# Optimization experiments

Measured on AMD Instinct MI355X. Metric: run time of the kernel, lower is better.

The kernel has to match this reference:

```python
import jax, jax.numpy as jnp
import numpy as np

B, N, E = 2, 2048, 1024   # batch, seq_len, embed_dim (= hidden_dim)
H, HD = 16, 64            # num_heads, head_dim


def setup_inputs() -> dict:
    key = jax.random.key(0)
    ks = jax.random.split(key, 6)
    w = lambda k: jax.random.normal(k, (E, E), jnp.float32) * 0.02
    return {
        "x": jax.random.normal(ks[0], (B, N, E), jnp.float32),
        "Wq": w(ks[1]), "bq": jnp.zeros((E,), jnp.float32),
        "Wk": w(ks[2]), "bk": jnp.zeros((E,), jnp.float32),
        "Wv": w(ks[3]), "bv": jnp.zeros((E,), jnp.float32),
        "Wu": w(ks[4]), "bu": jnp.zeros((E,), jnp.float32),
        "Wo": w(ks[5]), "bo": jnp.zeros((E,), jnp.float32),
        "ln_g": jnp.ones((E,), jnp.float32),
        "ln_b": jnp.zeros((E,), jnp.float32),
    }


def reference(x, Wq, bq, Wk, bk, Wv, bv, Wu, bu, Wo, bo, ln_g, ln_b):
    # projections (torch Linear: x @ W.T + b)
    q = x @ Wq.T + bq
    k = x @ Wk.T + bk
    v = jax.nn.silu(x @ Wv.T + bv)   # uv_act = swish
    u = jax.nn.silu(x @ Wu.T + bu)
    # split heads: [B, N, H*HD] -> [B, H, N, HD]
    split = lambda t: t.reshape(B, N, H, HD).transpose(0, 2, 1, 3)
    q, k, v = split(q), split(k), split(v)
    # non-softmax attention: ReLU on scaled energy (no causal mask)
    energy = jnp.einsum("bhnd,bhmd->bhnm", q, k) / jnp.float32(np.sqrt(HD))
    energy = jax.nn.relu(energy)
    out = jnp.einsum("bhnm,bhmd->bhnd", energy, v)
    # merge heads: [B, H, N, HD] -> [B, N, H*HD]
    out = out.transpose(0, 2, 1, 3).reshape(B, N, H * HD)
    # layernorm over hidden_dim
    mu = out.mean(-1, keepdims=True)
    var = out.var(-1, keepdims=True)
    out = (out - mu) * jax.lax.rsqrt(var + 1e-5) * ln_g + ln_b
    # gate and output projection
    out = u * out
    return out @ Wo.T + bo
```

## Files before the change

### kernel.cpp

```cpp
#include <hip/hip_runtime.h>
#include <stdint.h>

typedef unsigned short u16;
typedef __attribute__((ext_vector_type(8))) short short8;
typedef __attribute__((ext_vector_type(4))) short short4v;
typedef __attribute__((ext_vector_type(4))) float floatx4;
typedef __attribute__((ext_vector_type(4))) int intx4;

#define B_ 2
#define N_ 2048
#define E_ 1024
#define H_ 16
#define HD_ 64
#define M_TOT (B_ * N_)

__device__ __forceinline__ float bf2f(u16 h) {
    union { unsigned u; float f; } c; c.u = ((unsigned)h) << 16; return c.f;
}
__device__ __forceinline__ u16 f2bf(float f) {
    union { float f; unsigned u; } c; c.f = f;
    unsigned r = c.u + 0x7FFFu + ((c.u >> 16) & 1u);
    return (u16)(r >> 16);
}
__device__ __forceinline__ float silu_f(float x) { return x / (1.f + __expf(-x)); }

template <typename T> __device__ __forceinline__ void store_out(T* p, float v);
template <> __device__ __forceinline__ void store_out<u16>(u16* p, float v)    { *p = f2bf(v); }
template <> __device__ __forceinline__ void store_out<float>(float* p, float v) { *p = v; }

__device__ __forceinline__ void gll16(const void* g, void* l) {
    __builtin_amdgcn_global_load_lds(
        (const __attribute__((address_space(1))) void*)g,
        (__attribute__((address_space(3))) void*)l,
        16, 0, 0);
}

__launch_bounds__(256, 4)
__global__ void cvt_bf16(const float* __restrict__ src, u16* __restrict__ dst, int n)
{
    const int i = (blockIdx.x * 256 + threadIdx.x) * 8;
    if (i >= n) return;
    floatx4 a = *(const floatx4*)(src + i);
    floatx4 b = *(const floatx4*)(src + i + 4);
    union { u16 h[8]; intx4 v; } o;
    o.h[0] = f2bf(a[0]); o.h[1] = f2bf(a[1]); o.h[2] = f2bf(a[2]); o.h[3] = f2bf(a[3]);
    o.h[4] = f2bf(b[0]); o.h[5] = f2bf(b[1]); o.h[6] = f2bf(b[2]); o.h[7] = f2bf(b[3]);
    *(intx4*)(dst + i) = o.v;
}

__launch_bounds__(256, 4)
__global__ void cvt5(const float* __restrict__ s0, const float* __restrict__ s1,
                     const float* __restrict__ s2, const float* __restrict__ s3,
                     const float* __restrict__ s4,
                     u16* __restrict__ d0, u16* __restrict__ d1,
                     u16* __restrict__ d2, u16* __restrict__ d3,
                     u16* __restrict__ d4)
{
    const int z = blockIdx.z;
    const float* src = (z == 0) ? s0 : (z == 1) ? s1 : (z == 2) ? s2 : (z == 3) ? s3 : s4;
    u16* dst         = (z == 0) ? d0 : (z == 1) ? d1 : (z == 2) ? d2 : (z == 3) ? d3 : d4;
    const int i = (blockIdx.x * 256 + threadIdx.x) * 8;
    floatx4 a = *(const floatx4*)(src + i);
    floatx4 b = *(const floatx4*)(src + i + 4);
    union { u16 h[8]; intx4 v; } o;
    o.h[0] = f2bf(a[0]); o.h[1] = f2bf(a[1]); o.h[2] = f2bf(a[2]); o.h[3] = f2bf(a[3]);
    o.h[4] = f2bf(b[0]); o.h[5] = f2bf(b[1]); o.h[6] = f2bf(b[2]); o.h[7] = f2bf(b[3]);
    *(intx4*)(dst + i) = o.v;
}

template <typename OutT>
__launch_bounds__(256, 2)
__global__ void gemm4(const u16* __restrict__ A,
                      const u16* __restrict__ W0, const u16* __restrict__ W1,
                      const u16* __restrict__ W2, const u16* __restrict__ W3,
                      const float* __restrict__ bi0, const float* __restrict__ bi1,
                      const float* __restrict__ bi2, const float* __restrict__ bi3,
                      OutT* __restrict__ O0, OutT* __restrict__ O1,
                      OutT* __restrict__ O2, OutT* __restrict__ O3,
                      int actmask, int K)
{
    __shared__ u16 a_lds[128 * 32];
    __shared__ u16 b_lds[128 * 32];

    const int z = blockIdx.z;
    const u16* W    = (z == 0) ? W0 : (z == 1) ? W1 : (z == 2) ? W2 : W3;
    const float* Bi = (z == 0) ? bi0 : (z == 1) ? bi1 : (z == 2) ? bi2 : bi3;
    OutT* Out       = (z == 0) ? O0 : (z == 1) ? O1 : (z == 2) ? O2 : O3;
    const bool act = (actmask >> z) & 1;

    const int t    = threadIdx.x;
    const int wave = t >> 6, lane = t & 63, quad = lane >> 4, l16 = lane & 15;
    const int wm = wave >> 1, wn = wave & 1;
    const int m0 = blockIdx.y * 128;
    const int n0 = blockIdx.x * 128;

    floatx4 acc[4][4];
    const floatx4 fz = {0.f, 0.f, 0.f, 0.f};
    for (int i = 0; i < 4; i++)
        for (int j = 0; j < 4; j++) acc[i][j] = fz;

    const int ar = t >> 2;
    const int ac = (t & 3) * 8;
    const u16* Ag0 = A + (size_t)(m0 + ar) * K + ac;
    const u16* Ag1 = A + (size_t)(m0 + 64 + ar) * K + ac;
    const u16* Bg0 = W + (size_t)(n0 + ar) * K + ac;
    const u16* Bg1 = W + (size_t)(n0 + 64 + ar) * K + ac;
    u16* al0 = a_lds + wave * 512;
    u16* al1 = a_lds + 2048 + wave * 512;
    u16* bl0 = b_lds + wave * 512;
    u16* bl1 = b_lds + 2048 + wave * 512;

    for (int k0 = 0; k0 < K; k0 += 32) {
        __syncthreads();
        gll16(Ag0 + k0, al0);
        gll16(Ag1 + k0, al1);
        gll16(Bg0 + k0, bl0);
        gll16(Bg1 + k0, bl1);
        __syncthreads();

        short8 af[4], bfr[4];
        for (int i = 0; i < 4; i++)
            af[i]  = *(const short8*)&a_lds[(wm * 64 + i * 16 + l16) * 32 + quad * 8];
        for (int j = 0; j < 4; j++)
            bfr[j] = *(const short8*)&b_lds[(wn * 64 + j * 16 + l16) * 32 + quad * 8];
        for (int i = 0; i < 4; i++)
            for (int j = 0; j < 4; j++)
                acc[i][j] = __builtin_amdgcn_mfma_f32_16x16x32_bf16(af[i], bfr[j], acc[i][j], 0, 0, 0);
    }

    float bias_v[4];
    for (int j = 0; j < 4; j++) bias_v[j] = Bi[n0 + wn * 64 + j * 16 + l16];

    for (int i = 0; i < 4; i++) {
        const int row = m0 + wm * 64 + i * 16 + quad * 4;
        for (int j = 0; j < 4; j++) {
            const int col = n0 + wn * 64 + j * 16 + l16;
            for (int r = 0; r < 4; r++) {
                float v = acc[i][j][r] + bias_v[j];
                if (act) v = silu_f(v);
                store_out<OutT>(&Out[(size_t)(row + r) * E_ + col], v);
            }
        }
    }
}

__launch_bounds__(256, 4)
__global__ void vtrans(const u16* __restrict__ V, u16* __restrict__ VT)
{
    __shared__ u16 ts[64 * 72];
    const int bh = blockIdx.y;
    const int b = bh >> 4, h = bh & 15;
    const int n0 = blockIdx.x * 64;
    const int t = threadIdx.x;
    const int r = t >> 2, seg = (t & 3) * 16;

    const u16* src = V + ((size_t)b * N_ + n0 + r) * E_ + h * HD_ + seg;
    intx4 x0 = *(const intx4*)(src);
    intx4 x1 = *(const intx4*)(src + 8);
    *(intx4*)&ts[r * 72 + seg]     = x0;
    *(intx4*)&ts[r * 72 + seg + 8] = x1;
    __syncthreads();

    union { u16 h[16]; intx4 v[2]; } buf;
    for (int j = 0; j < 16; j++) buf.h[j] = ts[(seg + j) * 72 + r];
    u16* dst = VT + ((size_t)bh * HD_ + r) * N_ + n0 + seg;
    *(intx4*)(dst)     = buf.v[0];
    *(intx4*)(dst + 8) = buf.v[1];
}

#define LQ 72

__launch_bounds__(256, 2)
__global__ void attn(const u16* __restrict__ Q, const u16* __restrict__ Kk,
                     const u16* __restrict__ VT, float* __restrict__ Oa)
{
    __shared__ u16 k_lds[64 * LQ];
    __shared__ u16 vt_lds[64 * LQ];
    __shared__ u16 s_lds[4 * 32 * LQ];

    const int bh = blockIdx.y;
    const int b = bh >> 4, h = bh & 15;
    const int t = threadIdx.x;
    const int wave = t >> 6, lane = t & 63, quad = lane >> 4, l16 = lane & 15;
    const int q0 = blockIdx.x * 128 + wave * 32;
    const size_t base = (size_t)b * N_ * E_ + h * HD_;

    short8 aq[2][2];
    for (int mi = 0; mi < 2; mi++)
        for (int ks = 0; ks < 2; ks++)
            aq[mi][ks] = *(const short8*)(Q + base + (size_t)(q0 + mi * 16 + l16) * E_ + ks * 32 + quad * 8);

    floatx4 o[2][4];
    const floatx4 fz = {0.f, 0.f, 0.f, 0.f};
    for (int mi = 0; mi < 2; mi++)
        for (int n = 0; n < 4; n++) o[mi][n] = fz;

    const int srow = t >> 2;
    const int sseg = (t & 3) * 16;
    const u16* Ksrc = Kk + base + (size_t)srow * E_ + sseg;
    const u16* Vsrc = VT + ((size_t)bh * HD_ + srow) * N_ + sseg;

    u16* sw = &s_lds[wave * 32 * LQ];

    for (int kt = 0; kt < N_ / 64; kt++) {
        __syncthreads();
        intx4 k0v = *(const intx4*)(Ksrc + (size_t)(kt * 64) * E_);
        intx4 k1v = *(const intx4*)(Ksrc + (size_t)(kt * 64) * E_ + 8);
        intx4 v0v = *(const intx4*)(Vsrc + kt * 64);
        intx4 v1v = *(const intx4*)(Vsrc + kt * 64 + 8);
        *(intx4*)&k_lds[srow * LQ + sseg]      = k0v;
        *(intx4*)&k_lds[srow * LQ + sseg + 8]  = k1v;
        *(intx4*)&vt_lds[srow * LQ + sseg]     = v0v;
        *(intx4*)&vt_lds[srow * LQ + sseg + 8] = v1v;
        __syncthreads();

        short8 bk[4][2];
        for (int n = 0; n < 4; n++)
            for (int ks = 0; ks < 2; ks++)
                bk[n][ks] = *(const short8*)&k_lds[(n * 16 + l16) * LQ + ks * 32 + quad * 8];

        for (int mi = 0; mi < 2; mi++) {
            for (int n = 0; n < 4; n++) {
                floatx4 s = fz;
                for (int ks = 0; ks < 2; ks++)
                    s = __builtin_amdgcn_mfma_f32_16x16x32_bf16(aq[mi][ks], bk[n][ks], s, 0, 0, 0);
                for (int r = 0; r < 4; r++) {
                    float v = s[r] * 0.125f;
                    v = v > 0.f ? v : 0.f;
                    sw[(mi * 16 + quad * 4 + r) * LQ + n * 16 + l16] = f2bf(v);
                }
            }
        }

        for (int ks = 0; ks < 2; ks++) {
            short8 bv[4];
            for (int n = 0; n < 4; n++)
                bv[n] = *(const short8*)&vt_lds[(n * 16 + l16) * LQ + ks * 32 + quad * 8];
            for (int mi = 0; mi < 2; mi++) {
                short8 as = *(const short8*)&sw[(mi * 16 + l16) * LQ + ks * 32 + quad * 8];
                for (int n = 0; n < 4; n++)
                    o[mi][n] = __builtin_amdgcn_mfma_f32_16x16x32_bf16(as, bv[n], o[mi][n], 0, 0, 0);
            }
        }
    }

    for (int mi = 0; mi < 2; mi++)
        for (int n = 0; n < 4; n++)
            for (int r = 0; r < 4; r++)
                Oa[(size_t)(b * N_ + q0 + mi * 16 + quad * 4 + r) * E_ + h * HD_ + n * 16 + l16] = o[mi][n][r];
}

__launch_bounds__(256, 4)
__global__ void ln_gate(const float* __restrict__ A, const u16* __restrict__ U,
                        const float* __restrict__ G, const float* __restrict__ Bb,
                        u16* __restrict__ Out)
{
    const int row = blockIdx.x;
    const int t = threadIdx.x;
    const floatx4 v = *(const floatx4*)(A + (size_t)row * E_ + t * 4);
    float s  = v[0] + v[1] + v[2] + v[3];
    float ss = v[0] * v[0] + v[1] * v[1] + v[2] * v[2] + v[3] * v[3];
    for (int off = 32; off; off >>= 1) {
        s  += __shfl_down(s, off, 64);
        ss += __shfl_down(ss, off, 64);
    }
    __shared__ float red[8];
    const int wave = t >> 6, lane = t & 63;
    if (lane == 0) { red[wave] = s; red[4 + wave] = ss; }
    __syncthreads();
    const float S  = red[0] + red[1] + red[2] + red[3];
    const float SS = red[4] + red[5] + red[6] + red[7];
    const float mu  = S * (1.f / E_);
    const float var = SS * (1.f / E_) - mu * mu;
    const float rstd = rsqrtf(var + 1e-5f);

    short4v outv;
    for (int i = 0; i < 4; i++) {
        const int e = t * 4 + i;
        float y = (v[i] - mu) * rstd * G[e] + Bb[e];
        y *= bf2f(U[(size_t)row * E_ + e]);
        outv[i] = (short)f2bf(y);
    }
    *(short4v*)(Out + (size_t)row * E_ + t * 4) = outv;
}

extern "C" void kernel_launch(void* const* d_in, const int* in_sizes, int n_in,
                              void* d_out, int out_size, void* d_ws, size_t ws_size,
                              hipStream_t stream)
{
    const float* x   = (const float*)d_in[0];
    const float* Wq  = (const float*)d_in[1];
    const float* bq  = (const float*)d_in[2];
    const float* Wk  = (const float*)d_in[3];
    const float* bk  = (const float*)d_in[4];
    const float* Wv  = (const float*)d_in[5];
    const float* bv  = (const float*)d_in[6];
    const float* Wu  = (const float*)d_in[7];
    const float* bu  = (const float*)d_in[8];
    const float* Wo  = (const float*)d_in[9];
    const float* bo  = (const float*)d_in[10];
    const float* lng = (const float*)d_in[11];
    const float* lnb = (const float*)d_in[12];

    char* ws = (char*)d_ws;
    u16*  qw  = (u16*)(ws);
    u16*  kw  = (u16*)(ws + 8388608);
    u16*  vw  = (u16*)(ws + 16777216);
    u16*  uw  = (u16*)(ws + 25165824);
    float* aw = (float*)(ws + 33554432);
    u16*  xb  = (u16*)(ws + 50331648);
    u16*  vt  = (u16*)(ws + 50331648);
    u16*  wbq = (u16*)(ws + 58720256);
    u16*  wbk = (u16*)(ws + 60817408);
    u16*  wbv = (u16*)(ws + 62914560);
    u16*  wbu = (u16*)(ws + 65011712);
    u16*  wbo = (u16*)(ws + 67108864);
    u16*  gw  = (u16*)(ws);

    float* out = (float*)d_out;

    const dim3 blk(256, 1, 1);

    cvt_bf16<<<dim3(M_TOT * E_ / 2048, 1, 1), blk, 0, stream>>>(x, xb, M_TOT * E_);
    cvt5<<<dim3(E_ * E_ / 2048, 1, 5), blk, 0, stream>>>(Wq, Wk, Wv, Wu, Wo,
                                                         wbq, wbk, wbv, wbu, wbo);
    gemm4<u16><<<dim3(8, 32, 4), blk, 0, stream>>>(xb, wbq, wbk, wbv, wbu,
                                                   bq, bk, bv, bu,
                                                   qw, kw, vw, uw, 0xC, E_);
    vtrans<<<dim3(N_ / 64, B_ * H_, 1), blk, 0, stream>>>(vw, vt);
    attn<<<dim3(N_ / 128, B_ * H_, 1), blk, 0, stream>>>(qw, kw, vt, aw);
    ln_gate<<<dim3(M_TOT, 1, 1), blk, 0, stream>>>(aw, uw, lng, lnb, gw);
    gemm4<float><<<dim3(8, 32, 1), blk, 0, stream>>>(gw, wbo, wbo, wbo, wbo,
                                                     bo, bo, bo, bo,
                                                     out, out, out, out, 0x0, E_);
}
```

Baseline: 245.6 us.

## Split attention over key dimension and merge input/weight conversion kernels

```diff
diff --git a/kernel.cpp b/kernel.cpp
--- a/kernel.cpp
+++ b/kernel.cpp
@@ -36,29 +36,19 @@
 }
 
 __launch_bounds__(256, 4)
-__global__ void cvt_bf16(const float* __restrict__ src, u16* __restrict__ dst, int n)
-{
-    const int i = (blockIdx.x * 256 + threadIdx.x) * 8;
-    if (i >= n) return;
-    floatx4 a = *(const floatx4*)(src + i);
-    floatx4 b = *(const floatx4*)(src + i + 4);
-    union { u16 h[8]; intx4 v; } o;
-    o.h[0] = f2bf(a[0]); o.h[1] = f2bf(a[1]); o.h[2] = f2bf(a[2]); o.h[3] = f2bf(a[3]);
-    o.h[4] = f2bf(b[0]); o.h[5] = f2bf(b[1]); o.h[6] = f2bf(b[2]); o.h[7] = f2bf(b[3]);
-    *(intx4*)(dst + i) = o.v;
-}
-
-__launch_bounds__(256, 4)
-__global__ void cvt5(const float* __restrict__ s0, const float* __restrict__ s1,
+__global__ void cvt6(const float* __restrict__ s0, const float* __restrict__ s1,
                      const float* __restrict__ s2, const float* __restrict__ s3,
-                     const float* __restrict__ s4,
+                     const float* __restrict__ s4, const float* __restrict__ s5,
                      u16* __restrict__ d0, u16* __restrict__ d1,
                      u16* __restrict__ d2, u16* __restrict__ d3,
-                     u16* __restrict__ d4)
+                     u16* __restrict__ d4, u16* __restrict__ d5)
 {
     const int z = blockIdx.z;
-    const float* src = (z == 0) ? s0 : (z == 1) ? s1 : (z == 2) ? s2 : (z == 3) ? s3 : s4;
-    u16* dst         = (z == 0) ? d0 : (z == 1) ? d1 : (z == 2) ? d2 : (z == 3) ? d3 : d4;
+    if (z > 0 && blockIdx.x >= E_ * E_ / 2048) return;
+    const float* src = (z == 0) ? s0 : (z == 1) ? s1 : (z == 2) ? s2
+                     : (z == 3) ? s3 : (z == 4) ? s4 : s5;
+    u16* dst         = (z == 0) ? d0 : (z == 1) ? d1 : (z == 2) ? d2
+                     : (z == 3) ? d3 : (z == 4) ? d4 : d5;
     const int i = (blockIdx.x * 256 + threadIdx.x) * 8;
     floatx4 a = *(const floatx4*)(src + i);
     floatx4 b = *(const floatx4*)(src + i + 4);
@@ -169,10 +159,13 @@
 }
 
 #define LQ 72
+#define KSPLIT 2
+#define KCHUNK (N_ / KSPLIT)
 
 __launch_bounds__(256, 2)
 __global__ void attn(const u16* __restrict__ Q, const u16* __restrict__ Kk,
-                     const u16* __restrict__ VT, float* __restrict__ Oa)
+                     const u16* __restrict__ VT,
+                     float* __restrict__ Oa0, float* __restrict__ Oa1)
 {
     __shared__ u16 k_lds[64 * LQ];
     __shared__ u16 vt_lds[64 * LQ];
@@ -180,6 +173,10 @@
 
     const int bh = blockIdx.y;
     const int b = bh >> 4, h = bh & 15;
+    const int z = blockIdx.z;
+    float* __restrict__ Oa = (z == 0) ? Oa0 : Oa1;
+    const int key_base = z * KCHUNK;
+
     const int t = threadIdx.x;
     const int wave = t >> 6, lane = t & 63, quad = lane >> 4, l16 = lane & 15;
     const int q0 = blockIdx.x * 128 + wave * 32;
@@ -197,12 +194,12 @@
 
     const int srow = t >> 2;
     const int sseg = (t & 3) * 16;
-    const u16* Ksrc = Kk + base + (size_t)srow * E_ + sseg;
-    const u16* Vsrc = VT + ((size_t)bh * HD_ + srow) * N_ + sseg;
+    const u16* Ksrc = Kk + base + (size_t)(key_base + srow) * E_ + sseg;
+    const u16* Vsrc = VT + ((size_t)bh * HD_ + srow) * N_ + key_base + sseg;
 
     u16* sw = &s_lds[wave * 32 * LQ];
 
-    for (int kt = 0; kt < N_ / 64; kt++) {
+    for (int kt = 0; kt < KCHUNK / 64; kt++) {
         __syncthreads();
         intx4 k0v = *(const intx4*)(Ksrc + (size_t)(kt * 64) * E_);
         intx4 k1v = *(const intx4*)(Ksrc + (size_t)(kt * 64) * E_ + 8);
@@ -251,13 +248,17 @@
 }
 
 __launch_bounds__(256, 4)
-__global__ void ln_gate(const float* __restrict__ A, const u16* __restrict__ U,
+__global__ void ln_gate(const float* __restrict__ A0, const float* __restrict__ A1,
+                        const u16* __restrict__ U,
                         const float* __restrict__ G, const float* __restrict__ Bb,
                         u16* __restrict__ Out)
 {
     const int row = blockIdx.x;
     const int t = threadIdx.x;
-    const floatx4 v = *(const floatx4*)(A + (size_t)row * E_ + t * 4);
+    const floatx4 v0 = *(const floatx4*)(A0 + (size_t)row * E_ + t * 4);
+    const floatx4 v1 = *(const floatx4*)(A1 + (size_t)row * E_ + t * 4);
+    floatx4 v;
+    for (int i = 0; i < 4; i++) v[i] = v0[i] + v1[i];
     float s  = v[0] + v[1] + v[2] + v[3];
     float ss = v[0] * v[0] + v[1] * v[1] + v[2] * v[2] + v[3] * v[3];
     for (int off = 32; off; off >>= 1) {
@@ -321,15 +322,14 @@
 
     const dim3 blk(256, 1, 1);
 
-    cvt_bf16<<<dim3(M_TOT * E_ / 2048, 1, 1), blk, 0, stream>>>(x, xb, M_TOT * E_);
-    cvt5<<<dim3(E_ * E_ / 2048, 1, 5), blk, 0, stream>>>(Wq, Wk, Wv, Wu, Wo,
-                                                         wbq, wbk, wbv, wbu, wbo);
+    cvt6<<<dim3(M_TOT * E_ / 2048, 1, 6), blk, 0, stream>>>(
+        x, Wq, Wk, Wv, Wu, Wo, xb, wbq, wbk, wbv, wbu, wbo);
     gemm4<u16><<<dim3(8, 32, 4), blk, 0, stream>>>(xb, wbq, wbk, wbv, wbu,
                                                    bq, bk, bv, bu,
                                                    qw, kw, vw, uw, 0xC, E_);
     vtrans<<<dim3(N_ / 64, B_ * H_, 1), blk, 0, stream>>>(vw, vt);
-    attn<<<dim3(N_ / 128, B_ * H_, 1), blk, 0, stream>>>(qw, kw, vt, aw);
-    ln_gate<<<dim3(M_TOT, 1, 1), blk, 0, stream>>>(aw, uw, lng, lnb, gw);
+    attn<<<dim3(N_ / 128, B_ * H_, KSPLIT), blk, 0, stream>>>(qw, kw, vt, aw, out);
+    ln_gate<<<dim3(M_TOT, 1, 1), blk, 0, stream>>>(aw, out, uw, lng, lnb, gw);
     gemm4<float><<<dim3(8, 32, 1), blk, 0, stream>>>(gw, wbo, wbo, wbo, wbo,
                                                      bo, bo, bo, bo,
                                                      out, out, out, out, 0x0, E_);
```

Result: faster. 238.0 us (-3.1%).
